# Kernel optimization log

Measured on AMD Instinct MI355X. Metric: run time of the kernel, lower is better.

The kernel has to match this reference:

```python
import jax, jax.numpy as jnp
import numpy as np

NUM_HEADS = 16
HIDDEN = 1024
TOTAL = 2048
NSEG = 8


def setup_inputs() -> dict:
    key = jax.random.key(0)
    ks = jax.random.split(key, 10)
    x = jax.random.normal(ks[0], (TOTAL, HIDDEN), dtype=jnp.float32)
    # cu_seqlens: [0, b1, ..., TOTAL], sorted segment boundaries
    inner = np.sort(np.random.default_rng(0).integers(1, TOTAL, size=NSEG - 1))
    cu_seqlens = jnp.asarray(np.concatenate([[0], inner, [TOTAL]]), dtype=jnp.int32)
    s = 1.0 / np.sqrt(HIDDEN)
    def lin(k):
        kw, kb = jax.random.split(k)
        W = jax.random.uniform(kw, (HIDDEN, HIDDEN), jnp.float32, -s, s)
        b = jax.random.uniform(kb, (HIDDEN,), jnp.float32, -s, s)
        return W, b
    Wq, bq = lin(ks[1]); Wk, bk = lin(ks[2]); Wv, bv = lin(ks[3]); Wo, bo = lin(ks[4])
    return {"hidden_states_packed": x, "cu_seqlens": cu_seqlens,
            "Wq": Wq, "bq": bq, "Wk": Wk, "bk": bk,
            "Wv": Wv, "bv": bv, "Wo": Wo, "bo": bo}


def reference(hidden_states_packed, cu_seqlens, Wq, bq, Wk, bk, Wv, bv, Wo, bo):
    T, H = hidden_states_packed.shape
    dh = H // NUM_HEADS
    x = hidden_states_packed
    q = (x @ Wq.T + bq).reshape(T, NUM_HEADS, dh)
    k = (x @ Wk.T + bk).reshape(T, NUM_HEADS, dh)
    v = (x @ Wv.T + bv).reshape(T, NUM_HEADS, dh)
    # segment id of each token from cu_seqlens boundaries
    seg = jnp.searchsorted(cu_seqlens, jnp.arange(T, dtype=jnp.int32), side="right")
    same_seg = seg[:, None] == seg[None, :]  # [T, T] block-diagonal mask
    scale = 1.0 / jnp.sqrt(jnp.asarray(dh, x.dtype))
    scores = jnp.einsum("qhd,khd->hqk", q, k) * scale  # [H, T, T]
    neg = jnp.asarray(jnp.finfo(scores.dtype).min, scores.dtype)
    scores = jnp.where(same_seg[None, :, :], scores, neg)
    attn = jax.nn.softmax(scores, axis=-1)
    ctx = jnp.einsum("hqk,khd->qhd", attn, v).reshape(T, H)
    return ctx @ Wo.T + bo
```

## Files before the change

### kernel.cpp

```cpp
#include <hip/hip_runtime.h>

typedef _Float16 f16x8 __attribute__((ext_vector_type(8)));
typedef _Float16 f16x4 __attribute__((ext_vector_type(4)));
typedef float    f32x4 __attribute__((ext_vector_type(4)));

#define MFMA_F16(a, b, c) __builtin_amdgcn_mfma_f32_16x16x32_f16((a), (b), (c), 0, 0, 0)

typedef __attribute__((address_space(1))) void gas_void;
typedef __attribute__((address_space(3))) void las_void;
#define GLOAD_LDS16(g, l) \
  __builtin_amdgcn_global_load_lds((gas_void*)(g), (las_void*)(l), 16, 0, 0)

#define NEG_INF (-__builtin_inff())

constexpr int T_SEQ  = 2048;
constexpr int HID    = 1024;
constexpr int NHEADS = 16;
constexpr int DH     = 64;
constexpr int NSEG   = 8;

__global__ __launch_bounds__(256) void convert_all(
    const float* __restrict__ x,
    const float* __restrict__ Wq, const float* __restrict__ Wk,
    const float* __restrict__ Wv, const float* __restrict__ Wo,
    _Float16* __restrict__ xh,
    _Float16* __restrict__ Wqh, _Float16* __restrict__ Wkh,
    _Float16* __restrict__ Wvh, _Float16* __restrict__ Woh) {
  int i = blockIdx.x * 256 + threadIdx.x;
  const float* src;
  _Float16* dst;
  int local;
  if (i < 524288) {
    src = x; dst = xh; local = i;
  } else {
    int j = i - 524288;
    int w = j >> 18;
    local = j & 262143;
    src = (w == 0) ? Wq : (w == 1) ? Wk : (w == 2) ? Wv : Wo;
    dst = (w == 0) ? Wqh : (w == 1) ? Wkh : (w == 2) ? Wvh : Woh;
  }
  float4 f = *(const float4*)(src + (size_t)local * 4);
  f16x4 h;
  h[0] = (_Float16)f.x; h[1] = (_Float16)f.y;
  h[2] = (_Float16)f.z; h[3] = (_Float16)f.w;
  *(f16x4*)(dst + (size_t)local * 4) = h;
}

template <int LAYOUT, int BM>
__device__ __forceinline__ void gemm128(const _Float16* __restrict__ A,
                                        const _Float16* __restrict__ B,
                                        const float* __restrict__ bias,
                                        _Float16* __restrict__ outh,
                                        float* __restrict__ outf) {
  constexpr int K = HID, N = HID;
  constexpr int MI = BM / 32;
  constexpr int LA = (BM * 8) / 512;
  __shared__ _Float16 As[BM * 64];
  __shared__ _Float16 Bs[128 * 64];
  const int tid  = threadIdx.x;
  const int wave = tid >> 6, lane = tid & 63;
  const int lr = lane & 15, lq = lane >> 4;
  const int wm = (wave >> 2) * (BM / 2);
  const int wn = (wave & 3) * 32;
  const int bm = blockIdx.y * BM, bn = blockIdx.x * 128;

  const _Float16* gA[LA > 0 ? LA : 1];
  const _Float16* gB[2];
  _Float16* lA[LA > 0 ? LA : 1];
  _Float16* lB[2];
#pragma unroll
  for (int i = 0; i < LA; ++i) {
    const int s = i * 512 + tid;
    const int row = s >> 3, pch = s & 7;
    const int lch = pch ^ (row & 7);
    gA[i] = A + (size_t)(bm + row) * K + lch * 8;
    lA[i] = &As[(i * 512 + wave * 64) * 8];
  }
#pragma unroll
  for (int i = 0; i < 2; ++i) {
    const int s = i * 512 + tid;
    const int row = s >> 3, pch = s & 7;
    const int lch = pch ^ (row & 7);
    gB[i] = B + (size_t)(bn + row) * K + lch * 8;
    lB[i] = &Bs[(i * 512 + wave * 64) * 8];
  }

  f32x4 acc[MI][2] = {};

  for (int kk = 0; kk < K; kk += 64) {
#pragma unroll
    for (int i = 0; i < LA; ++i) GLOAD_LDS16(gA[i] + kk, lA[i]);
#pragma unroll
    for (int i = 0; i < 2; ++i) GLOAD_LDS16(gB[i] + kk, lB[i]);
    __syncthreads();
#pragma unroll
    for (int ks = 0; ks < 2; ++ks) {
      f16x8 af[MI], bf[2];
#pragma unroll
      for (int mi = 0; mi < MI; ++mi) {
        const int row = wm + mi * 16 + lr;
        af[mi] = *(const f16x8*)&As[row * 64 + (((ks * 4 + lq) ^ (row & 7)) * 8)];
      }
#pragma unroll
      for (int ni = 0; ni < 2; ++ni) {
        const int row = wn + ni * 16 + lr;
        bf[ni] = *(const f16x8*)&Bs[row * 64 + (((ks * 4 + lq) ^ (row & 7)) * 8)];
      }
#pragma unroll
      for (int mi = 0; mi < MI; ++mi)
#pragma unroll
        for (int ni = 0; ni < 2; ++ni)
          acc[mi][ni] = MFMA_F16(af[mi], bf[ni], acc[mi][ni]);
    }
    __syncthreads();
  }

#pragma unroll
  for (int ni = 0; ni < 2; ++ni) {
    const int col = bn + wn + ni * 16 + lr;
    const float bv = bias[col];
#pragma unroll
    for (int mi = 0; mi < MI; ++mi) {
      const f32x4 v = acc[mi][ni];
      const int row0 = bm + wm + mi * 16 + lq * 4;
      if (LAYOUT == 3) {
        f16x4 o;
#pragma unroll
        for (int r = 0; r < 4; ++r) o[r] = (_Float16)(v[r] + bv);
        *(f16x4*)&outh[(size_t)col * T_SEQ + row0] = o;
      } else {
#pragma unroll
        for (int r = 0; r < 4; ++r) {
          const int row = row0 + r;
          const float val = v[r] + bv;
          if (LAYOUT == 0)
            outh[((size_t)(col >> 6) * T_SEQ + row) * DH + (col & 63)] = (_Float16)val;
          else
            outf[(size_t)row * N + col] = val;
        }
      }
    }
  }
}

__global__ __launch_bounds__(512) void gemm_qkv(
    const _Float16* __restrict__ xh,
    const _Float16* __restrict__ Wqh, const _Float16* __restrict__ Wkh,
    const _Float16* __restrict__ Wvh,
    const float* __restrict__ bq, const float* __restrict__ bk,
    const float* __restrict__ bv,
    _Float16* __restrict__ qp, _Float16* __restrict__ kp,
    _Float16* __restrict__ vT) {
  const int z = blockIdx.z;
  if (z == 0) {
    gemm128<0, 128>(xh, Wqh, bq, qp, nullptr);
  } else if (z == 1) {
    gemm128<0, 128>(xh, Wkh, bk, kp, nullptr);
  } else {
    gemm128<3, 128>(xh, Wvh, bv, vT, nullptr);
  }
}

__global__ __launch_bounds__(512) void gemm_out(
    const _Float16* __restrict__ ctxh, const _Float16* __restrict__ Woh,
    const float* __restrict__ bo, float* __restrict__ out) {
  gemm128<1, 64>(ctxh, Woh, bo, nullptr, out);
}

__device__ __forceinline__ float redsum16(float v) {
  v += __shfl_xor(v, 1);
  v += __shfl_xor(v, 2);
  v += __shfl_xor(v, 4);
  v += __shfl_xor(v, 8);
  return v;
}

__global__ __launch_bounds__(512, 4) void attn_kernel(
    const _Float16* __restrict__ qp, const _Float16* __restrict__ kp,
    const _Float16* __restrict__ vT, const int* __restrict__ cu,
    _Float16* __restrict__ ctx) {
  constexpr float SCL2E = 0.125f * 1.44269504f;
  constexpr int PSTR = 72;
  __shared__ _Float16 Ks[2][64 * 64];
  __shared__ _Float16 Vs[2][64 * 64];
  __shared__ _Float16 Pl[8][16 * PSTR];
  float* mO = (float*)&Ks[0][0];
  float* mL = (float*)&Vs[0][0];
  const int h  = blockIdx.x & 15;
  const int q0 = (blockIdx.x >> 4) * 64;
  const int tid = threadIdx.x, wave = tid >> 6, lane = tid & 63;
  const int lr = lane & 15, lq = lane >> 4;
  const int qsub = wave & 3, khalf = wave >> 2;
  const int qw = q0 + qsub * 16;

  int cs[NSEG + 1];
#pragma unroll
  for (int i = 0; i <= NSEG; ++i) cs[i] = cu[i];

  int sstart[4], send[4];
#pragma unroll
  for (int r = 0; r < 4; ++r) {
    const int row = qw + lq * 4 + r;
    sstart[r] = 0; send[r] = T_SEQ;
#pragma unroll
    for (int s = 0; s < NSEG; ++s)
      if (row >= cs[s] && row < cs[s + 1]) { sstart[r] = cs[s]; send[r] = cs[s + 1]; }
  }
  int wlo = 0, whi = T_SEQ, wlo2 = 0;
#pragma unroll
  for (int s = 0; s < NSEG; ++s) {
    if (qw >= cs[s] && qw < cs[s + 1]) { wlo = cs[s]; whi = cs[s + 1]; }
    if (qw + 15 >= cs[s] && qw + 15 < cs[s + 1]) wlo2 = cs[s];
  }
  const bool wsame = (wlo == wlo2);
  int klo = 0, khi = T_SEQ;
#pragma unroll
  for (int s = 0; s < NSEG; ++s) {
    if (q0 >= cs[s] && q0 < cs[s + 1]) klo = cs[s];
    if (q0 + 63 >= cs[s] && q0 + 63 < cs[s + 1]) khi = cs[s + 1];
  }
  klo &= ~63;
  const int range  = khi - klo;
  const int hlen   = ((range + 127) >> 7) << 6;
  const int nsteps = hlen >> 6;
  const int kstart = klo + khalf * hlen;

  const _Float16* qbase = qp + ((size_t)h * T_SEQ + qw + lr) * DH;
  f16x8 qf0 = *(const f16x8*)(qbase + lq * 8);
  f16x8 qf1 = *(const f16x8*)(qbase + 32 + lq * 8);
#pragma unroll
  for (int i = 0; i < 8; ++i) {
    qf0[i] = qf0[i] * (_Float16)SCL2E;
    qf1[i] = qf1[i] * (_Float16)SCL2E;
  }

  const _Float16* kb = kp + (size_t)h * T_SEQ * DH;
  const _Float16* vb = vT + (size_t)h * DH * T_SEQ;

  const int ht = qsub * 64 + lane;
  int kRow[2], kCol[2], vRow[2], vCol[2];
  _Float16* lK[2];
  _Float16* lV[2];
#pragma unroll
  for (int i = 0; i < 2; ++i) {
    const int s = i * 256 + ht;
    const int row = s >> 3, pch = s & 7;
    const int lch = pch ^ (row & 7);
    kRow[i] = row; kCol[i] = lch * 8;
    vRow[i] = row; vCol[i] = lch * 8;
    lK[i] = &Ks[khalf][(i * 256 + qsub * 64) * 8];
    lV[i] = &Vs[khalf][(i * 256 + qsub * 64) * 8];
  }

  float lst[4] = {0.f, 0.f, 0.f, 0.f};
  f32x4 oacc[4];
#pragma unroll
  for (int c = 0; c < 4; ++c) oacc[c] = f32x4{0.f, 0.f, 0.f, 0.f};

  _Float16* pw = &Pl[wave][0];

  for (int s = 0; s < nsteps; ++s) {
    const int kt = kstart + s * 64;
#pragma unroll
    for (int i = 0; i < 2; ++i) {
      const int grow = min(kt + kRow[i], T_SEQ - 1);
      GLOAD_LDS16(kb + (size_t)grow * DH + kCol[i], lK[i]);
    }
#pragma unroll
    for (int i = 0; i < 2; ++i) {
      const int gcol = min(kt + vCol[i], T_SEQ - 8);
      GLOAD_LDS16(vb + (size_t)vRow[i] * T_SEQ + gcol, lV[i]);
    }
    __syncthreads();

    f32x4 sc[4];
#pragma unroll
    for (int n = 0; n < 4; ++n) {
      const int row = n * 16 + lr;
      const f16x8 kf0 =
          *(const f16x8*)&Ks[khalf][row * 64 + (((0 * 4 + lq) ^ (row & 7)) * 8)];
      const f16x8 kf1 =
          *(const f16x8*)&Ks[khalf][row * 64 + (((1 * 4 + lq) ^ (row & 7)) * 8)];
      sc[n] = f32x4{0.f, 0.f, 0.f, 0.f};
      sc[n] = MFMA_F16(qf0, kf0, sc[n]);
      sc[n] = MFMA_F16(qf1, kf1, sc[n]);
    }
    const bool fastTile = wsame && (kt >= wlo) && (kt + 64 <= whi);
    if (fastTile) {
#pragma unroll
      for (int r = 0; r < 4; ++r) {
        float p[4];
#pragma unroll
        for (int n = 0; n < 4; ++n) p[n] = exp2f(sc[n][r]);
        lst[r] += (p[0] + p[1]) + (p[2] + p[3]);
        _Float16* pr = &pw[(lq * 4 + r) * PSTR + lr];
        pr[0]  = (_Float16)p[0];
        pr[16] = (_Float16)p[1];
        pr[32] = (_Float16)p[2];
        pr[48] = (_Float16)p[3];
      }
    } else {
#pragma unroll
      for (int r = 0; r < 4; ++r) {
        float p[4];
#pragma unroll
        for (int n = 0; n < 4; ++n) {
          const int col = kt + n * 16 + lr;
          const float vv =
              (col >= sstart[r] && col < send[r]) ? sc[n][r] : NEG_INF;
          p[n] = exp2f(vv);
        }
        lst[r] += (p[0] + p[1]) + (p[2] + p[3]);
        _Float16* pr = &pw[(lq * 4 + r) * PSTR + lr];
        pr[0]  = (_Float16)p[0];
        pr[16] = (_Float16)p[1];
        pr[32] = (_Float16)p[2];
        pr[48] = (_Float16)p[3];
      }
    }
    const f16x8 pf0 = *(const f16x8*)&pw[lr * PSTR + lq * 8];
    const f16x8 pf1 = *(const f16x8*)&pw[lr * PSTR + 32 + lq * 8];
#pragma unroll
    for (int c = 0; c < 4; ++c) {
      const int row = c * 16 + lr;
      const f16x8 vf0 =
          *(const f16x8*)&Vs[khalf][row * 64 + (((0 * 4 + lq) ^ (row & 7)) * 8)];
      const f16x8 vf1 =
          *(const f16x8*)&Vs[khalf][row * 64 + (((1 * 4 + lq) ^ (row & 7)) * 8)];
      oacc[c] = MFMA_F16(pf0, vf0, oacc[c]);
      oacc[c] = MFMA_F16(pf1, vf1, oacc[c]);
    }
    __syncthreads();
  }

#pragma unroll
  for (int r = 0; r < 4; ++r) lst[r] = redsum16(lst[r]);

  if (khalf) {
#pragma unroll
    for (int c = 0; c < 4; ++c)
#pragma unroll
      for (int r = 0; r < 4; ++r)
        mO[((qsub * 16) + lq * 4 + r) * 64 + c * 16 + lr] = oacc[c][r];
    if (lr == 0) {
#pragma unroll
      for (int r = 0; r < 4; ++r) mL[qsub * 16 + lq * 4 + r] = lst[r];
    }
  }
  __syncthreads();
  if (!khalf) {
#pragma unroll
    for (int r = 0; r < 4; ++r) lst[r] += mL[qsub * 16 + lq * 4 + r];
#pragma unroll
    for (int c = 0; c < 4; ++c)
#pragma unroll
      for (int r = 0; r < 4; ++r) {
        const int row = qw + lq * 4 + r;
        const float val =
            (oacc[c][r] + mO[((qsub * 16) + lq * 4 + r) * 64 + c * 16 + lr]) /
            lst[r];
        ctx[(size_t)row * HID + h * DH + c * 16 + lr] = (_Float16)val;
      }
  }
}

extern "C" void kernel_launch(void* const* d_in, const int* in_sizes, int n_in,
                              void* d_out, int out_size, void* d_ws, size_t ws_size,
                              hipStream_t stream) {
  const float* x  = (const float*)d_in[0];
  const int* cu   = (const int*)d_in[1];
  const float* Wq = (const float*)d_in[2]; const float* bq = (const float*)d_in[3];
  const float* Wk = (const float*)d_in[4]; const float* bk = (const float*)d_in[5];
  const float* Wv = (const float*)d_in[6]; const float* bv = (const float*)d_in[7];
  const float* Wo = (const float*)d_in[8]; const float* bo = (const float*)d_in[9];
  float* out = (float*)d_out;

  char* ws = (char*)d_ws;
  _Float16* xh   = (_Float16*)(ws + (size_t)0);
  _Float16* Wqh  = (_Float16*)(ws + ((size_t)4 << 20));
  _Float16* Wkh  = (_Float16*)(ws + ((size_t)6 << 20));
  _Float16* Wvh  = (_Float16*)(ws + ((size_t)8 << 20));
  _Float16* Woh  = (_Float16*)(ws + ((size_t)10 << 20));
  _Float16* qp   = (_Float16*)(ws + ((size_t)12 << 20));
  _Float16* kp   = (_Float16*)(ws + ((size_t)16 << 20));
  _Float16* vT   = (_Float16*)(ws + ((size_t)20 << 20));
  _Float16* ctxh = (_Float16*)(ws + ((size_t)24 << 20));

  convert_all<<<6144, 256, 0, stream>>>(x, Wq, Wk, Wv, Wo, xh, Wqh, Wkh, Wvh, Woh);
  gemm_qkv<<<dim3(8, 16, 3), 512, 0, stream>>>(xh, Wqh, Wkh, Wvh, bq, bk, bv, qp, kp, vT);
  attn_kernel<<<512, 512, 0, stream>>>(qp, kp, vT, cu, ctxh);
  gemm_out<<<dim3(8, 32), 512, 0, stream>>>(ctxh, Woh, bo, out);
}
```

Before: 138.9 us.

## Double-buffer GEMM LDS tiles and raise wave priority around attention MFMAs

```diff
diff --git a/kernel.cpp b/kernel.cpp
--- a/kernel.cpp
+++ b/kernel.cpp
@@ -55,8 +55,9 @@
   constexpr int K = HID, N = HID;
   constexpr int MI = BM / 32;
   constexpr int LA = (BM * 8) / 512;
-  __shared__ _Float16 As[BM * 64];
-  __shared__ _Float16 Bs[128 * 64];
+  constexpr int NT = K / 64;
+  __shared__ _Float16 As[2][BM * 64];
+  __shared__ _Float16 Bs[2][128 * 64];
   const int tid  = threadIdx.x;
   const int wave = tid >> 6, lane = tid & 63;
   const int lr = lane & 15, lq = lane >> 4;
@@ -66,15 +67,15 @@
 
   const _Float16* gA[LA > 0 ? LA : 1];
   const _Float16* gB[2];
-  _Float16* lA[LA > 0 ? LA : 1];
-  _Float16* lB[2];
+  int oA[LA > 0 ? LA : 1];
+  int oB[2];
 #pragma unroll
   for (int i = 0; i < LA; ++i) {
     const int s = i * 512 + tid;
     const int row = s >> 3, pch = s & 7;
     const int lch = pch ^ (row & 7);
     gA[i] = A + (size_t)(bm + row) * K + lch * 8;
-    lA[i] = &As[(i * 512 + wave * 64) * 8];
+    oA[i] = (i * 512 + wave * 64) * 8;
   }
 #pragma unroll
   for (int i = 0; i < 2; ++i) {
@@ -82,29 +83,30 @@
     const int row = s >> 3, pch = s & 7;
     const int lch = pch ^ (row & 7);
     gB[i] = B + (size_t)(bn + row) * K + lch * 8;
-    lB[i] = &Bs[(i * 512 + wave * 64) * 8];
+    oB[i] = (i * 512 + wave * 64) * 8;
   }
 
   f32x4 acc[MI][2] = {};
 
-  for (int kk = 0; kk < K; kk += 64) {
-#pragma unroll
-    for (int i = 0; i < LA; ++i) GLOAD_LDS16(gA[i] + kk, lA[i]);
-#pragma unroll
-    for (int i = 0; i < 2; ++i) GLOAD_LDS16(gB[i] + kk, lB[i]);
-    __syncthreads();
+  auto stage = [&](int b, int kk) {
+#pragma unroll
+    for (int i = 0; i < LA; ++i) GLOAD_LDS16(gA[i] + kk, &As[b][oA[i]]);
+#pragma unroll
+    for (int i = 0; i < 2; ++i) GLOAD_LDS16(gB[i] + kk, &Bs[b][oB[i]]);
+  };
+  auto compute = [&](int b) {
 #pragma unroll
     for (int ks = 0; ks < 2; ++ks) {
       f16x8 af[MI], bf[2];
 #pragma unroll
       for (int mi = 0; mi < MI; ++mi) {
         const int row = wm + mi * 16 + lr;
-        af[mi] = *(const f16x8*)&As[row * 64 + (((ks * 4 + lq) ^ (row & 7)) * 8)];
+        af[mi] = *(const f16x8*)&As[b][row * 64 + (((ks * 4 + lq) ^ (row & 7)) * 8)];
       }
 #pragma unroll
       for (int ni = 0; ni < 2; ++ni) {
         const int row = wn + ni * 16 + lr;
-        bf[ni] = *(const f16x8*)&Bs[row * 64 + (((ks * 4 + lq) ^ (row & 7)) * 8)];
+        bf[ni] = *(const f16x8*)&Bs[b][row * 64 + (((ks * 4 + lq) ^ (row & 7)) * 8)];
       }
 #pragma unroll
       for (int mi = 0; mi < MI; ++mi)
@@ -112,8 +114,17 @@
         for (int ni = 0; ni < 2; ++ni)
           acc[mi][ni] = MFMA_F16(af[mi], bf[ni], acc[mi][ni]);
     }
+  };
+
+  stage(0, 0);
+  __syncthreads();
+#pragma unroll
+  for (int t = 1; t < NT; ++t) {
+    stage(t & 1, t * 64);
+    compute((t & 1) ^ 1);
     __syncthreads();
   }
+  compute((NT - 1) & 1);
 
 #pragma unroll
   for (int ni = 0; ni < 2; ++ni) {
@@ -274,6 +285,7 @@
     __syncthreads();
 
     f32x4 sc[4];
+    __builtin_amdgcn_s_setprio(1);
 #pragma unroll
     for (int n = 0; n < 4; ++n) {
       const int row = n * 16 + lr;
@@ -285,6 +297,7 @@
       sc[n] = MFMA_F16(qf0, kf0, sc[n]);
       sc[n] = MFMA_F16(qf1, kf1, sc[n]);
     }
+    __builtin_amdgcn_s_setprio(0);
     const bool fastTile = wsame && (kt >= wlo) && (kt + 64 <= whi);
     if (fastTile) {
 #pragma unroll
@@ -320,6 +333,7 @@
     }
     const f16x8 pf0 = *(const f16x8*)&pw[lr * PSTR + lq * 8];
     const f16x8 pf1 = *(const f16x8*)&pw[lr * PSTR + 32 + lq * 8];
+    __builtin_amdgcn_s_setprio(1);
 #pragma unroll
     for (int c = 0; c < 4; ++c) {
       const int row = c * 16 + lr;
@@ -330,6 +344,7 @@
       oacc[c] = MFMA_F16(pf0, vf0, oacc[c]);
       oacc[c] = MFMA_F16(pf1, vf1, oacc[c]);
     }
+    __builtin_amdgcn_s_setprio(0);
     __syncthreads();
   }
 
```

Result: slower. 151.2 us (+8.8%).
